# Kernel tuning notes

Measured on AMD Instinct MI355X. Metric: run time of the kernel, lower is better.

Reference implementation:

```python
import jax, jax.numpy as jnp
import numpy as np

D_K = 128  # query/key dim, used for the 1/sqrt(d_k) scale


def setup_inputs() -> dict:
    key = jax.random.key(0)
    k1, k2, k3, k4 = jax.random.split(key, 4)
    B, L, d_model, d_k, d_v = 4, 2048, 1024, 128, 128

    def xavier(k, shape):
        # matches nn.init.xavier_uniform_ for 2D weights
        limit = np.sqrt(6.0 / (shape[0] + shape[1]))
        return jax.random.uniform(k, shape, jnp.float32, -limit, limit)

    return {
        "X": jax.random.normal(k1, (B, L, d_model), jnp.float32),
        "W_Q": xavier(k2, (d_model, d_k)),
        "W_K": xavier(k3, (d_model, d_k)),
        "W_V": xavier(k4, (d_model, d_v)),
    }


def reference(X, W_Q, W_K, W_V):
    # X: (B, L, d_model)
    L = X.shape[1]
    Q = jnp.einsum("bld,dk->blk", X, W_Q)          # (B, L, d_k)
    K = jnp.einsum("bld,dk->blk", X, W_K)          # (B, L, d_k)
    V = jnp.einsum("bld,dv->blv", X, W_V)          # (B, L, d_v)
    scale = D_K ** -0.5
    scores = jnp.einsum("bqk,bpk->bqp", Q, K) * scale  # (B, L, L)
    # causal mask: positions above the diagonal set to -inf
    causal = jnp.tril(jnp.ones((L, L), dtype=bool))
    scores = jnp.where(causal, scores, -jnp.inf)
    A = jax.nn.softmax(scores, axis=-1)            # (B, L, L)
    Z = jnp.einsum("bqp,bpv->bqv", A, V)           # (B, L, d_v)
    return Z
```

## Files before the change

### kernel.cpp

```cpp
#include <hip/hip_runtime.h>
#include <hip/hip_bf16.h>

typedef __bf16 bf16;
typedef __attribute__((ext_vector_type(4))) __bf16 bf16x4;
typedef __attribute__((ext_vector_type(8))) __bf16 bf16x8;
typedef __attribute__((ext_vector_type(4))) float f32x4;

#define D_MODEL 1024
#define DK 128
#define LSEQ 2048
#define NQT 128
#define NB 4
#define SCALE2 (0.08838834764831845f * 1.4426950408889634f)

__global__ __launch_bounds__(256) void wt_kernel(
    const float* __restrict__ Wq, const float* __restrict__ Wk,
    const float* __restrict__ Wv, bf16* __restrict__ Wt)
{
    __shared__ bf16 tile[64][72];
    const float* W = (blockIdx.z == 0) ? Wq : (blockIdx.z == 1) ? Wk : Wv;
    int k0 = blockIdx.x * 64;
    int n0 = blockIdx.y * 64;
    int t  = threadIdx.x;
    #pragma unroll
    for (int i = 0; i < 16; ++i) {
        int idx = t + i * 256;
        int r = idx >> 6, c = idx & 63;
        tile[c][r] = (bf16)W[(size_t)(k0 + r) * DK + n0 + c];
    }
    __syncthreads();
    bf16* out = Wt + (size_t)blockIdx.z * DK * D_MODEL;
    #pragma unroll
    for (int i = 0; i < 16; ++i) {
        int idx = t + i * 256;
        int rr = idx >> 6, cc = idx & 63;
        out[(size_t)(n0 + rr) * D_MODEL + k0 + cc] = tile[rr][cc];
    }
}

__global__ __launch_bounds__(256) void proj_kernel(
    const float* __restrict__ X, const bf16* __restrict__ Wt,
    bf16* __restrict__ Qs, bf16* __restrict__ Kb, bf16* __restrict__ Vt)
{
    __shared__ bf16 Xs[64][72];
    __shared__ bf16 Ws[128][72];
    int mt = blockIdx.x, mat = blockIdx.y;
    const bf16* W = Wt + (size_t)mat * DK * D_MODEL;
    int t = threadIdx.x;
    int wave = t >> 6, lane = t & 63;
    int lq = lane & 15, g = lane >> 4;
    int row0 = mt * 64;

    f32x4 acc[4][2];
    #pragma unroll
    for (int m = 0; m < 4; ++m)
        #pragma unroll
        for (int n = 0; n < 2; ++n) acc[m][n] = f32x4{0.f, 0.f, 0.f, 0.f};

    f32x4  rxf[4];
    bf16x8 rw[4];
    auto LOADR = [&](int k0) {
        #pragma unroll
        for (int i = 0; i < 4; ++i) {
            int u = t + i * 256, r = u >> 4, c4 = u & 15;
            rxf[i] = *reinterpret_cast<const f32x4*>(
                &X[(size_t)(row0 + r) * D_MODEL + k0 + c4 * 4]);
        }
        #pragma unroll
        for (int i = 0; i < 4; ++i) {
            int u = t + i * 256, r = u >> 3, c8 = u & 7;
            rw[i] = *reinterpret_cast<const bf16x8*>(
                &W[(size_t)r * D_MODEL + k0 + c8 * 8]);
        }
    };
    auto STORER = [&]() {
        #pragma unroll
        for (int i = 0; i < 4; ++i) {
            int u = t + i * 256, r = u >> 4, c4 = u & 15;
            bf16x4 h;
            h[0]=(bf16)rxf[i][0]; h[1]=(bf16)rxf[i][1];
            h[2]=(bf16)rxf[i][2]; h[3]=(bf16)rxf[i][3];
            *reinterpret_cast<bf16x4*>(&Xs[r][c4 * 4]) = h;
        }
        #pragma unroll
        for (int i = 0; i < 4; ++i) {
            int u = t + i * 256, r = u >> 3, c8 = u & 7;
            *reinterpret_cast<bf16x8*>(&Ws[r][c8 * 8]) = rw[i];
        }
    };

    LOADR(0);
    for (int ks = 0; ks < 16; ++ks) {
        __syncthreads();
        STORER();
        if (ks + 1 < 16) LOADR((ks + 1) * 64);
        __syncthreads();
        #pragma unroll
        for (int kk = 0; kk < 2; ++kk) {
            bf16x8 a[4];
            #pragma unroll
            for (int mr = 0; mr < 4; ++mr)
                a[mr] = *reinterpret_cast<const bf16x8*>(&Xs[mr * 16 + lq][kk * 32 + g * 8]);
            #pragma unroll
            for (int n = 0; n < 2; ++n) {
                bf16x8 bfr = *reinterpret_cast<const bf16x8*>(
                    &Ws[wave * 32 + n * 16 + lq][kk * 32 + g * 8]);
                #pragma unroll
                for (int mr = 0; mr < 4; ++mr)
                    acc[mr][n] = __builtin_amdgcn_mfma_f32_16x16x32_bf16(a[mr], bfr, acc[mr][n], 0, 0, 0);
            }
        }
    }
    #pragma unroll
    for (int mr = 0; mr < 4; ++mr) {
        int orow = row0 + mr * 16 + g * 4;
        #pragma unroll
        for (int n = 0; n < 2; ++n) {
            int col = wave * 32 + n * 16 + lq;
            if (mat == 0) {
                #pragma unroll
                for (int r = 0; r < 4; ++r)
                    Qs[(size_t)(orow + r) * DK + col] = (bf16)(acc[mr][n][r] * SCALE2);
            } else if (mat == 1) {
                #pragma unroll
                for (int r = 0; r < 4; ++r)
                    Kb[(size_t)(orow + r) * DK + col] = (bf16)acc[mr][n][r];
            } else {
                int bb  = orow >> 11;
                int kv0 = orow & 2047;
                bf16x4 h;
                h[0]=(bf16)acc[mr][n][0]; h[1]=(bf16)acc[mr][n][1];
                h[2]=(bf16)acc[mr][n][2]; h[3]=(bf16)acc[mr][n][3];
                *reinterpret_cast<bf16x4*>(
                    &Vt[((size_t)bb * DK + col) * LSEQ + kv0]) = h;
            }
        }
    }
}

__global__ __launch_bounds__(256, 3) void attn_kernel(
    const bf16* __restrict__ Qs, const bf16* __restrict__ Kb,
    const bf16* __restrict__ Vt, float* __restrict__ Zp,
    float* __restrict__ Mp, float* __restrict__ Lp,
    float* __restrict__ Out, int split)
{
    __shared__ bf16 Ks[64][136];
    __shared__ bf16 Vs[128][72];
    __shared__ bf16 P[4][16][72];
    int bid = blockIdx.x;
    int b, qblk, s;
    if (split) {
        int xcd = bid & 7, u = bid >> 3;
        b = xcd >> 1;
        int n2 = (u << 1) | (xcd & 1);
        int q = 0, off = 0;
        while (off + ((q >> 2) + 1) <= n2) { off += (q >> 2) + 1; ++q; }
        qblk = q;
        s = n2 - off;
    } else {
        b = bid >> 5;
        qblk = bid & 31;
        s = 0;
    }
    int t = threadIdx.x;
    int wave = t >> 6, lane = t & 63;
    int lq = lane & 15, g = lane >> 4;
    int qw16 = qblk * 4 + wave;
    int qg = qw16 * 16 + lq;

    int nt = qblk + 1;
    int t0 = split ? 4 * s : 0;
    int t1 = split ? min(4 * s + 4, nt) : nt;

    const bf16* Kbase = Kb + (size_t)b * LSEQ * DK;
    const bf16* Vbase = Vt + (size_t)b * DK * LSEQ;

    const bf16* Qrow = Qs + ((size_t)b * LSEQ + qg) * DK;
    bf16x8 qf[4];
    #pragma unroll
    for (int ks = 0; ks < 4; ++ks)
        qf[ks] = *reinterpret_cast<const bf16x8*>(&Qrow[ks * 32 + g * 8]);

    f32x4 z[8];
    #pragma unroll
    for (int i = 0; i < 8; ++i) z[i] = f32x4{0.f, 0.f, 0.f, 0.f};
    float mrun = -3.0e38f, lrun = 0.f;

    bf16x8 kreg[4], vreg[4];
    auto LOADKV = [&](int kvb) {
        #pragma unroll
        for (int i = 0; i < 4; ++i) {
            int u = t + i * 256, r = u >> 4, c = u & 15;
            kreg[i] = *reinterpret_cast<const bf16x8*>(
                &Kbase[(size_t)(kvb + r) * DK + c * 8]);
        }
        #pragma unroll
        for (int i = 0; i < 4; ++i) {
            int u = t + i * 256, d = u >> 3, c = u & 7;
            vreg[i] = *reinterpret_cast<const bf16x8*>(
                &Vbase[(size_t)d * LSEQ + kvb + c * 8]);
        }
    };
    auto STOREKV = [&]() {
        #pragma unroll
        for (int i = 0; i < 4; ++i) {
            int u = t + i * 256, r = u >> 4, c = u & 15;
            *reinterpret_cast<bf16x8*>(&Ks[r][c * 8]) = kreg[i];
        }
        #pragma unroll
        for (int i = 0; i < 4; ++i) {
            int u = t + i * 256, d = u >> 3, c = u & 7;
            *reinterpret_cast<bf16x8*>(&Vs[d][c * 8]) = vreg[i];
        }
    };

    LOADKV(t0 * 64);
    for (int ti = t0; ti < t1; ++ti) {
        int kvb = ti * 64;
        __syncthreads();
        STOREKV();
        if (ti + 1 < t1) LOADKV((ti + 1) * 64);
        __syncthreads();

        f32x4 sc[4];
        #pragma unroll
        for (int jj = 0; jj < 4; ++jj) sc[jj] = f32x4{0.f, 0.f, 0.f, 0.f};
        __builtin_amdgcn_s_setprio(1);
        #pragma unroll
        for (int jj = 0; jj < 4; ++jj)
            #pragma unroll
            for (int ks = 0; ks < 4; ++ks) {
                bf16x8 a = *reinterpret_cast<const bf16x8*>(
                    &Ks[jj * 16 + lq][ks * 32 + g * 8]);
                sc[jj] = __builtin_amdgcn_mfma_f32_16x16x32_bf16(a, qf[ks], sc[jj], 0, 0, 0);
            }
        __builtin_amdgcn_s_setprio(0);

        float sv[16];
        if (ti == nt - 1) {
            #pragma unroll
            for (int jj = 0; jj < 4; ++jj)
                #pragma unroll
                for (int r = 0; r < 4; ++r) {
                    int kv0 = kvb + jj * 16 + g * 4 + r;
                    sv[jj * 4 + r] = (kv0 <= qg) ? sc[jj][r] : -3.0e38f;
                }
        } else {
            #pragma unroll
            for (int jj = 0; jj < 4; ++jj)
                #pragma unroll
                for (int r = 0; r < 4; ++r) sv[jj * 4 + r] = sc[jj][r];
        }
        float mt = sv[0];
        #pragma unroll
        for (int i = 1; i < 16; ++i) mt = fmaxf(mt, sv[i]);
        mt = fmaxf(mt, __shfl_xor(mt, 16));
        mt = fmaxf(mt, __shfl_xor(mt, 32));
        if (!__all(mt <= mrun)) {
            float mnew  = fmaxf(mrun, mt);
            float alpha = exp2f(mrun - mnew);
            lrun *= alpha;
            #pragma unroll
            for (int i = 0; i < 8; ++i) {
                z[i][0] *= alpha; z[i][1] *= alpha; z[i][2] *= alpha; z[i][3] *= alpha;
            }
            mrun = mnew;
        }
        float psum = 0.f;
        #pragma unroll
        for (int jj = 0; jj < 4; ++jj) {
            bf16x4 pb;
            #pragma unroll
            for (int r = 0; r < 4; ++r) {
                float e = exp2f(sv[jj * 4 + r] - mrun);
                psum += e;
                pb[r] = (bf16)e;
            }
            *reinterpret_cast<bf16x4*>(&P[wave][lq][jj * 16 + g * 4]) = pb;
        }
        psum += __shfl_xor(psum, 16);
        psum += __shfl_xor(psum, 32);
        lrun += psum;
        __builtin_amdgcn_s_setprio(1);
        #pragma unroll
        for (int sl = 0; sl < 2; ++sl) {
            bf16x8 pf = *reinterpret_cast<const bf16x8*>(&P[wave][lq][sl * 32 + g * 8]);
            #pragma unroll
            for (int dt = 0; dt < 8; ++dt) {
                bf16x8 av = *reinterpret_cast<const bf16x8*>(
                    &Vs[dt * 16 + lq][sl * 32 + g * 8]);
                z[dt] = __builtin_amdgcn_mfma_f32_16x16x32_bf16(av, pf, z[dt], 0, 0, 0);
            }
        }
        __builtin_amdgcn_s_setprio(0);
    }

    if (!split) {
        float inv = 1.f / lrun;
        float* orow = Out + ((size_t)b * LSEQ + qg) * DK;
        #pragma unroll
        for (int dt = 0; dt < 8; ++dt) {
            f32x4 v;
            v[0]=z[dt][0]*inv; v[1]=z[dt][1]*inv; v[2]=z[dt][2]*inv; v[3]=z[dt][3]*inv;
            *reinterpret_cast<f32x4*>(&orow[dt * 16 + g * 4]) = v;
        }
    } else {
        size_t T = ((size_t)(b * NQT + qw16) * 8 + s);
        float* zp = Zp + T * (16 * 128);
        #pragma unroll
        for (int dt = 0; dt < 8; ++dt)
            *reinterpret_cast<f32x4*>(&zp[lq * 128 + dt * 16 + g * 4]) = z[dt];
        if (g == 0) {
            Mp[T * 16 + lq] = mrun;
            Lp[T * 16 + lq] = lrun;
        }
    }
}

__global__ __launch_bounds__(256) void combine_kernel(
    const float* __restrict__ Zp, const float* __restrict__ Mp,
    const float* __restrict__ Lp, float* __restrict__ Out)
{
    int qt = blockIdx.x, b = blockIdx.y;
    int S  = (qt >> 4) + 1;
    int t  = threadIdx.x;
    int r  = t >> 4;
    int d0 = (t & 15) * 8;
    size_t Tbase = (size_t)(b * NQT + qt) * 8;

    float m = -3.0e38f;
    for (int s = 0; s < S; ++s)
        m = fmaxf(m, Mp[(Tbase + s) * 16 + r]);

    float L = 0.f;
    f32x4 a0 = {0.f,0.f,0.f,0.f}, a1 = {0.f,0.f,0.f,0.f};
    for (int s = 0; s < S; ++s) {
        float w = exp2f(Mp[(Tbase + s) * 16 + r] - m);
        L += w * Lp[(Tbase + s) * 16 + r];
        const float* zp = Zp + (Tbase + s) * (16 * 128) + r * 128 + d0;
        f32x4 v0 = *reinterpret_cast<const f32x4*>(&zp[0]);
        f32x4 v1 = *reinterpret_cast<const f32x4*>(&zp[4]);
        a0[0]+=w*v0[0]; a0[1]+=w*v0[1]; a0[2]+=w*v0[2]; a0[3]+=w*v0[3];
        a1[0]+=w*v1[0]; a1[1]+=w*v1[1]; a1[2]+=w*v1[2]; a1[3]+=w*v1[3];
    }
    float inv = 1.f / L;
    float* orow = Out + ((size_t)b * LSEQ + qt * 16 + r) * DK + d0;
    f32x4 o0, o1;
    o0[0]=a0[0]*inv; o0[1]=a0[1]*inv; o0[2]=a0[2]*inv; o0[3]=a0[3]*inv;
    o1[0]=a1[0]*inv; o1[1]=a1[1]*inv; o1[2]=a1[2]*inv; o1[3]=a1[3]*inv;
    *reinterpret_cast<f32x4*>(&orow[0]) = o0;
    *reinterpret_cast<f32x4*>(&orow[4]) = o1;
}

extern "C" void kernel_launch(void* const* d_in, const int* in_sizes, int n_in,
                              void* d_out, int out_size, void* d_ws, size_t ws_size,
                              hipStream_t stream)
{
    const float* X  = (const float*)d_in[0];
    const float* Wq = (const float*)d_in[1];
    const float* Wk = (const float*)d_in[2];
    const float* Wv = (const float*)d_in[3];
    float* Out = (float*)d_out;

    char* ws = (char*)d_ws;
    bf16* Wt = (bf16*)(ws);
    bf16* Qs = (bf16*)(ws + ((size_t)1 << 20));
    bf16* Kb = (bf16*)(ws + ((size_t)3 << 20));
    bf16* Vt = (bf16*)(ws + ((size_t)5 << 20));
    size_t base = (size_t)7 << 20;

    size_t zp_bytes = (size_t)NB * NQT * 8 * 16 * 128 * 4;
    size_t ml_bytes = (size_t)NB * NQT * 8 * 16 * 4;
    int split = (ws_size >= base + zp_bytes + 2 * ml_bytes) ? 1 : 0;

    float* Zp = (float*)(ws + base);
    float* Mp = (float*)(ws + base + zp_bytes);
    float* Lp = (float*)(ws + base + zp_bytes + ml_bytes);

    hipLaunchKernelGGL(wt_kernel,   dim3(16, 2, 3), dim3(256), 0, stream, Wq, Wk, Wv, Wt);
    hipLaunchKernelGGL(proj_kernel, dim3(128, 3),   dim3(256), 0, stream, X, Wt, Qs, Kb, Vt);
    hipLaunchKernelGGL(attn_kernel, dim3(split ? 576 : NB * 32), dim3(256), 0, stream,
                       Qs, Kb, Vt, Zp, Mp, Lp, Out, split);
    if (split)
        hipLaunchKernelGGL(combine_kernel, dim3(NQT, NB), dim3(256), 0, stream,
                           Zp, Mp, Lp, Out);
}
```

Measured before the change: 51.88 us.

## Double-buffer projection with direct-to-LDS W loads and store split partials in bf16

```diff
diff --git a/kernel.cpp b/kernel.cpp
--- a/kernel.cpp
+++ b/kernel.cpp
@@ -12,6 +12,10 @@
 #define NQT 128
 #define NB 4
 #define SCALE2 (0.08838834764831845f * 1.4426950408889634f)
+
+#define GLD16(g, l) __builtin_amdgcn_global_load_lds(                       \
+    (const __attribute__((address_space(1))) void*)(g),                     \
+    (__attribute__((address_space(3))) void*)(l), 16, 0, 0)
 
 __global__ __launch_bounds__(256) void wt_kernel(
     const float* __restrict__ Wq, const float* __restrict__ Wk,
@@ -42,14 +46,15 @@
     const float* __restrict__ X, const bf16* __restrict__ Wt,
     bf16* __restrict__ Qs, bf16* __restrict__ Kb, bf16* __restrict__ Vt)
 {
-    __shared__ bf16 Xs[64][72];
-    __shared__ bf16 Ws[128][72];
+    __shared__ bf16 Xs[2][64][72];
+    __shared__ __align__(16) bf16 Ws[2][128][64];
     int mt = blockIdx.x, mat = blockIdx.y;
     const bf16* W = Wt + (size_t)mat * DK * D_MODEL;
     int t = threadIdx.x;
     int wave = t >> 6, lane = t & 63;
     int lq = lane & 15, g = lane >> 4;
     int row0 = mt * 64;
+    int key8 = lq & 7;
 
     f32x4 acc[4][2];
     #pragma unroll
@@ -57,59 +62,67 @@
         #pragma unroll
         for (int n = 0; n < 2; ++n) acc[m][n] = f32x4{0.f, 0.f, 0.f, 0.f};
 
-    f32x4  rxf[4];
-    bf16x8 rw[4];
-    auto LOADR = [&](int k0) {
+    f32x4 rxf[4];
+    auto LOADX = [&](int k0) {
         #pragma unroll
         for (int i = 0; i < 4; ++i) {
             int u = t + i * 256, r = u >> 4, c4 = u & 15;
             rxf[i] = *reinterpret_cast<const f32x4*>(
                 &X[(size_t)(row0 + r) * D_MODEL + k0 + c4 * 4]);
         }
-        #pragma unroll
-        for (int i = 0; i < 4; ++i) {
-            int u = t + i * 256, r = u >> 3, c8 = u & 7;
-            rw[i] = *reinterpret_cast<const bf16x8*>(
-                &W[(size_t)r * D_MODEL + k0 + c8 * 8]);
-        }
     };
-    auto STORER = [&]() {
+    auto STOREX = [&](int buf) {
         #pragma unroll
         for (int i = 0; i < 4; ++i) {
             int u = t + i * 256, r = u >> 4, c4 = u & 15;
             bf16x4 h;
             h[0]=(bf16)rxf[i][0]; h[1]=(bf16)rxf[i][1];
             h[2]=(bf16)rxf[i][2]; h[3]=(bf16)rxf[i][3];
-            *reinterpret_cast<bf16x4*>(&Xs[r][c4 * 4]) = h;
-        }
-        #pragma unroll
-        for (int i = 0; i < 4; ++i) {
-            int u = t + i * 256, r = u >> 3, c8 = u & 7;
-            *reinterpret_cast<bf16x8*>(&Ws[r][c8 * 8]) = rw[i];
+            *reinterpret_cast<bf16x4*>(&Xs[buf][r][c4 * 4]) = h;
         }
     };
-
-    LOADR(0);
+    auto GLDW = [&](int k0, int buf) {
+        #pragma unroll
+        for (int i = 0; i < 4; ++i) {
+            int e = t + i * 256;
+            int r = e >> 3, c = e & 7;
+            const char* gsrc = (const char*)W +
+                (((size_t)r * D_MODEL) + k0 + ((c ^ (r & 7)) << 3)) * 2;
+            char* ldst = (char*)(&Ws[buf][0][0]) + (size_t)e * 16;
+            GLD16(gsrc, ldst);
+        }
+    };
+
+    GLDW(0, 0);
+    LOADX(0);
+    STOREX(0);
+    __syncthreads();
+
+    int b = 0;
     for (int ks = 0; ks < 16; ++ks) {
-        __syncthreads();
-        STORER();
-        if (ks + 1 < 16) LOADR((ks + 1) * 64);
-        __syncthreads();
+        if (ks + 1 < 16) {
+            GLDW((ks + 1) * 64, b ^ 1);
+            LOADX((ks + 1) * 64);
+        }
         #pragma unroll
         for (int kk = 0; kk < 2; ++kk) {
             bf16x8 a[4];
             #pragma unroll
             for (int mr = 0; mr < 4; ++mr)
-                a[mr] = *reinterpret_cast<const bf16x8*>(&Xs[mr * 16 + lq][kk * 32 + g * 8]);
+                a[mr] = *reinterpret_cast<const bf16x8*>(
+                    &Xs[b][mr * 16 + lq][kk * 32 + g * 8]);
             #pragma unroll
             for (int n = 0; n < 2; ++n) {
                 bf16x8 bfr = *reinterpret_cast<const bf16x8*>(
-                    &Ws[wave * 32 + n * 16 + lq][kk * 32 + g * 8]);
+                    &Ws[b][wave * 32 + n * 16 + lq][((4 * kk + g) ^ key8) << 3]);
                 #pragma unroll
                 for (int mr = 0; mr < 4; ++mr)
                     acc[mr][n] = __builtin_amdgcn_mfma_f32_16x16x32_bf16(a[mr], bfr, acc[mr][n], 0, 0, 0);
             }
         }
+        if (ks + 1 < 16) STOREX(b ^ 1);
+        __syncthreads();
+        b ^= 1;
     }
     #pragma unroll
     for (int mr = 0; mr < 4; ++mr) {
@@ -140,7 +153,7 @@
 
 __global__ __launch_bounds__(256, 3) void attn_kernel(
     const bf16* __restrict__ Qs, const bf16* __restrict__ Kb,
-    const bf16* __restrict__ Vt, float* __restrict__ Zp,
+    const bf16* __restrict__ Vt, bf16* __restrict__ Zp,
     float* __restrict__ Mp, float* __restrict__ Lp,
     float* __restrict__ Out, int split)
 {
@@ -306,10 +319,14 @@
         }
     } else {
         size_t T = ((size_t)(b * NQT + qw16) * 8 + s);
-        float* zp = Zp + T * (16 * 128);
-        #pragma unroll
-        for (int dt = 0; dt < 8; ++dt)
-            *reinterpret_cast<f32x4*>(&zp[lq * 128 + dt * 16 + g * 4]) = z[dt];
+        bf16* zp = Zp + T * (16 * 128);
+        #pragma unroll
+        for (int dt = 0; dt < 8; ++dt) {
+            bf16x4 h;
+            h[0]=(bf16)z[dt][0]; h[1]=(bf16)z[dt][1];
+            h[2]=(bf16)z[dt][2]; h[3]=(bf16)z[dt][3];
+            *reinterpret_cast<bf16x4*>(&zp[lq * 128 + dt * 16 + g * 4]) = h;
+        }
         if (g == 0) {
             Mp[T * 16 + lq] = mrun;
             Lp[T * 16 + lq] = lrun;
@@ -318,7 +335,7 @@
 }
 
 __global__ __launch_bounds__(256) void combine_kernel(
-    const float* __restrict__ Zp, const float* __restrict__ Mp,
+    const bf16* __restrict__ Zp, const float* __restrict__ Mp,
     const float* __restrict__ Lp, float* __restrict__ Out)
 {
     int qt = blockIdx.x, b = blockIdx.y;
@@ -333,21 +350,20 @@
         m = fmaxf(m, Mp[(Tbase + s) * 16 + r]);
 
     float L = 0.f;
-    f32x4 a0 = {0.f,0.f,0.f,0.f}, a1 = {0.f,0.f,0.f,0.f};
+    float a[8] = {0.f, 0.f, 0.f, 0.f, 0.f, 0.f, 0.f, 0.f};
     for (int s = 0; s < S; ++s) {
         float w = exp2f(Mp[(Tbase + s) * 16 + r] - m);
         L += w * Lp[(Tbase + s) * 16 + r];
-        const float* zp = Zp + (Tbase + s) * (16 * 128) + r * 128 + d0;
-        f32x4 v0 = *reinterpret_cast<const f32x4*>(&zp[0]);
-        f32x4 v1 = *reinterpret_cast<const f32x4*>(&zp[4]);
-        a0[0]+=w*v0[0]; a0[1]+=w*v0[1]; a0[2]+=w*v0[2]; a0[3]+=w*v0[3];
-        a1[0]+=w*v1[0]; a1[1]+=w*v1[1]; a1[2]+=w*v1[2]; a1[3]+=w*v1[3];
+        bf16x8 v = *reinterpret_cast<const bf16x8*>(
+            &Zp[(Tbase + s) * (16 * 128) + r * 128 + d0]);
+        #pragma unroll
+        for (int j = 0; j < 8; ++j) a[j] += w * (float)v[j];
     }
     float inv = 1.f / L;
     float* orow = Out + ((size_t)b * LSEQ + qt * 16 + r) * DK + d0;
     f32x4 o0, o1;
-    o0[0]=a0[0]*inv; o0[1]=a0[1]*inv; o0[2]=a0[2]*inv; o0[3]=a0[3]*inv;
-    o1[0]=a1[0]*inv; o1[1]=a1[1]*inv; o1[2]=a1[2]*inv; o1[3]=a1[3]*inv;
+    o0[0]=a[0]*inv; o0[1]=a[1]*inv; o0[2]=a[2]*inv; o0[3]=a[3]*inv;
+    o1[0]=a[4]*inv; o1[1]=a[5]*inv; o1[2]=a[6]*inv; o1[3]=a[7]*inv;
     *reinterpret_cast<f32x4*>(&orow[0]) = o0;
     *reinterpret_cast<f32x4*>(&orow[4]) = o1;
 }
@@ -369,11 +385,11 @@
     bf16* Vt = (bf16*)(ws + ((size_t)5 << 20));
     size_t base = (size_t)7 << 20;
 
-    size_t zp_bytes = (size_t)NB * NQT * 8 * 16 * 128 * 4;
+    size_t zp_bytes = (size_t)NB * NQT * 8 * 16 * 128 * 2;
     size_t ml_bytes = (size_t)NB * NQT * 8 * 16 * 4;
     int split = (ws_size >= base + zp_bytes + 2 * ml_bytes) ? 1 : 0;
 
-    float* Zp = (float*)(ws + base);
+    bf16*  Zp = (bf16*)(ws + base);
     float* Mp = (float*)(ws + base + zp_bytes);
     float* Lp = (float*)(ws + base + zp_bytes + ml_bytes);
 
```

Result: slower. 56.43 us (+8.8%).
